# Kernel optimization log

Measured on AMD Instinct MI355X. Metric: run time of the kernel, lower is better.

Reference implementation:

```python
import jax, jax.numpy as jnp
import numpy as np

B, N, E, HID, ED, NH = 2, 10000, 160000, 128, 32, 8
HD = HID // NH  # head_dim = 16
EPS = 1e-5


def setup_inputs() -> dict:
    key = jax.random.key(0)
    ks = jax.random.split(key, 12)
    s = 0.05  # keep pre-tanh activations in a sane range
    return {
        "h": jax.random.normal(ks[0], (B, N, HID), jnp.float32),
        "edge_attr": jax.random.normal(ks[1], (B, E, ED), jnp.float32),
        "edge_index": jax.random.randint(ks[2], (E, 2), 0, N),
        "Wq": jax.random.normal(ks[3], (HID, HID), jnp.float32) * s,
        "bq": jnp.zeros((HID,), jnp.float32),
        "Wk": jax.random.normal(ks[4], (HID, HID), jnp.float32) * s,
        "bk": jnp.zeros((HID,), jnp.float32),
        "Wv": jax.random.normal(ks[5], (HID, HID), jnp.float32) * s,
        "bv": jnp.zeros((HID,), jnp.float32),
        "We": jax.random.normal(ks[6], (HID, ED), jnp.float32) * s,
        "be": jnp.zeros((HID,), jnp.float32),
        "attn_vec": jax.random.normal(ks[7], (NH, HD), jnp.float32) * 0.02,
        "Ws": jax.random.normal(ks[8], (HID, HID), jnp.float32) * s,
        "bs": jnp.zeros((HID,), jnp.float32),
        "Wa": jax.random.normal(ks[9], (HID, HID), jnp.float32) * s,
        "ba": jnp.zeros((HID,), jnp.float32),
        "ln_g": jnp.ones((HID,), jnp.float32),
        "ln_b": jnp.zeros((HID,), jnp.float32),
    }


def reference(h, edge_attr, edge_index, Wq, bq, Wk, bk, Wv, bv, We, be,
              attn_vec, Ws, bs, Wa, ba, ln_g, ln_b):
    src = edge_index[:, 0]
    dst = edge_index[:, 1]
    b, n, hid = h.shape
    e_cnt = src.shape[0]

    h_src = h[:, src, :]  # [B,E,HID]
    h_dst = h[:, dst, :]

    q = (h_dst @ Wq.T + bq).reshape(b, e_cnt, NH, HD)
    k = (h_src @ Wk.T + bk).reshape(b, e_cnt, NH, HD)
    v = (h_src @ Wv.T + bv).reshape(b, e_cnt, NH, HD)
    e = (edge_attr @ We.T + be).reshape(b, e_cnt, NH, HD)

    # GATv2-style scores: [B,E,NH]
    logits = jnp.einsum('behd,hd->beh', jnp.tanh(q + k + e), attn_vec)
    logits = logits / np.float32(np.sqrt(HD))

    # segment softmax over edges grouped by dst node (stable)
    lt = jnp.transpose(logits, (1, 0, 2))  # [E,B,NH]
    mx = jax.ops.segment_max(lt, dst, num_segments=n)  # [N,B,NH]
    ex = jnp.exp(lt - mx[dst])
    den = jax.ops.segment_sum(ex, dst, num_segments=n)
    alpha = jnp.transpose(ex / den[dst], (1, 0, 2))  # [B,E,NH]

    msg = (alpha[..., None] * (v + e)).reshape(b, e_cnt, hid)  # [B,E,HID]
    agg = jax.ops.segment_sum(jnp.transpose(msg, (1, 0, 2)), dst, num_segments=n)
    agg = jnp.transpose(agg, (1, 0, 2))  # [B,N,HID]

    update = (h @ Ws.T + bs) + (agg @ Wa.T + ba)
    x = h + jax.nn.gelu(update, approximate=False)  # dropout is identity in eval

    mu = jnp.mean(x, axis=-1, keepdims=True)
    var = jnp.var(x, axis=-1, keepdims=True)
    return (x - mu) / jnp.sqrt(var + EPS) * ln_g + ln_b
```

## Files before the change

### kernel.cpp

```cpp
#include <hip/hip_runtime.h>
#include <math.h>
#include <stdint.h>

#define B_   2
#define N_   10000
#define E_   160000
#define HID_ 128
#define ED_  32
#define NH_  8
#define HD_  16
#define ROWS_ (B_ * N_)

using half2_t = __attribute__((ext_vector_type(2))) _Float16;
using f16x8   = __attribute__((ext_vector_type(8))) _Float16;
using f32x4   = __attribute__((ext_vector_type(4))) float;

__device__ __forceinline__ half2_t f2h2(float a, float b) {
    return __builtin_bit_cast(half2_t, __builtin_amdgcn_cvt_pkrtz(a, b));
}
__device__ __forceinline__ uint32_t pkh2(float a, float b) {
    return __builtin_bit_cast(uint32_t, __builtin_amdgcn_cvt_pkrtz(a, b));
}


__global__ void hist_kernel(const int* __restrict__ ei, int* __restrict__ deg, int E) {
    int e = blockIdx.x * 256 + threadIdx.x;
    if (e < E) atomicAdd(&deg[ei[2 * e + 1]], 1);
}

__global__ __launch_bounds__(256) void scan_kernel(const int* __restrict__ deg,
                                                   int* __restrict__ off, int N) {
    __shared__ int sums[256];
    int t = threadIdx.x;
    int chunk = (N + 255) / 256;
    int s0 = t * chunk, s1 = min(N, s0 + chunk);
    int s = 0;
    for (int i = s0; i < s1; ++i) s += deg[i];
    sums[t] = s;
    __syncthreads();
    #pragma unroll
    for (int d = 1; d < 256; d <<= 1) {
        int v = (t >= d) ? sums[t - d] : 0;
        __syncthreads();
        sums[t] += v;
        __syncthreads();
    }
    if (t == 255) off[N] = sums[255];
    int run = sums[t] - s;
    for (int i = s0; i < s1; ++i) { off[i] = run; run += deg[i]; }
}

__global__ void fill_kernel(const int* __restrict__ ei, const int* __restrict__ off,
                            int* __restrict__ cursor, int* __restrict__ csr,
                            int* __restrict__ srcs, int E) {
    int e = blockIdx.x * 256 + threadIdx.x;
    if (e < E) {
        int2 se = *(const int2*)(ei + 2 * e);
        int p = atomicAdd(&cursor[se.y], 1);
        int o = off[se.y] + p;
        csr[o] = e;
        srcs[o] = se.x;
    }
}


#define GM 64
#define LDA 68

__global__ __launch_bounds__(256) void qkvs_kernel(
    const float* __restrict__ h,
    const float* __restrict__ Wq, const float* __restrict__ bq,
    const float* __restrict__ Wk, const float* __restrict__ bk,
    const float* __restrict__ Wv, const float* __restrict__ bv,
    const float* __restrict__ Ws, const float* __restrict__ bs,
    const float* __restrict__ ba,
    float* __restrict__ Q, float* __restrict__ KV, float* __restrict__ S)
{
    __shared__ uint32_t As[GM * LDA];
    __shared__ uint32_t Bs[128 * LDA];
    __shared__ float bsm[128];

    int tid = threadIdx.x;
    int lane = tid & 63;
    int wave = tid >> 6;
    int row0 = blockIdx.x * GM;
    int J0 = blockIdx.y * 128;

    if (tid < 128) {
        int J = J0 + tid;
        float v;
        if (J < 128)      v = bq[J];
        else if (J < 256) v = bk[J - 128];
        else if (J < 384) v = bv[J - 256];
        else              v = bs[J - 384] + ba[J - 384];
        bsm[tid] = v;
    }

    for (int f = tid; f < GM * 32; f += 256) {
        int r = f >> 5, c4 = f & 31;
        long row = row0 + r;
        float4 hv = (row < ROWS_) ? *(const float4*)(h + row * HID_ + c4 * 4)
                                  : make_float4(0.f, 0.f, 0.f, 0.f);
        As[r * LDA + c4 * 2]     = pkh2(hv.x, hv.y);
        As[r * LDA + c4 * 2 + 1] = pkh2(hv.z, hv.w);
    }
    for (int f = tid; f < 128 * 32; f += 256) {
        int jr = f >> 5, c4 = f & 31;
        int J = J0 + jr;
        const float* Wp;
        if (J < 128)      Wp = Wq + (long)J * HID_;
        else if (J < 256) Wp = Wk + (long)(J - 128) * HID_;
        else if (J < 384) Wp = Wv + (long)(J - 256) * HID_;
        else              Wp = Ws + (long)(J - 384) * HID_;
        float4 wv = *(const float4*)(Wp + c4 * 4);
        Bs[jr * LDA + c4 * 2]     = pkh2(wv.x, wv.y);
        Bs[jr * LDA + c4 * 2 + 1] = pkh2(wv.z, wv.w);
    }
    __syncthreads();

    f32x4 acc[8];
    #pragma unroll
    for (int nt = 0; nt < 8; ++nt) {
        float c = bsm[nt * 16 + (lane & 15)];
        acc[nt] = (f32x4){ c, c, c, c };
    }

    int ar = wave * 16 + (lane & 15);
    #pragma unroll
    for (int ks = 0; ks < 4; ++ks) {
        f16x8 a = *(const f16x8*)(As + ar * LDA + ks * 16 + (lane >> 4) * 4);
        #pragma unroll
        for (int nt = 0; nt < 8; ++nt) {
            f16x8 b = *(const f16x8*)(Bs + (nt * 16 + (lane & 15)) * LDA + ks * 16 + (lane >> 4) * 4);
            acc[nt] = __builtin_amdgcn_mfma_f32_16x16x32_f16(a, b, acc[nt], 0, 0, 0);
        }
    }

    #pragma unroll
    for (int nt = 0; nt < 8; ++nt) {
        int J = J0 + nt * 16 + (lane & 15);
        long rbase = row0 + wave * 16 + (lane >> 4) * 4;
        #pragma unroll
        for (int r = 0; r < 4; ++r) {
            long row = rbase + r;
            if (row < ROWS_) {
                float v = acc[nt][r];
                if (J < 128)      Q[row * 128 + J] = v;
                else if (J < 256) KV[row * 256 + 2 * (J - 128)] = v;
                else if (J < 384) KV[row * 256 + 2 * (J - 256) + 1] = v;
                else              S[row * 128 + (J - 384)] = v;
            }
        }
    }
}


template <int CTRL>
__device__ __forceinline__ float dpp_add(float x) {
    int y = __builtin_amdgcn_mov_dpp(__float_as_int(x), CTRL, 0xF, 0xF, true);
    return x + __int_as_float(y);
}
__device__ __forceinline__ float hsum16(float p) {
    p = dpp_add<0xB1>(p);
    p = dpp_add<0x4E>(p);
    p = dpp_add<0x141>(p);
    p = dpp_add<0x140>(p);
    return p;
}


#define NPB 4
#define CHUNK 96
#define EAS 20

__global__ __launch_bounds__(128) void node_kernel(
    const float* __restrict__ edge_attr,
    const float* __restrict__ Q, const float* __restrict__ KV,
    const float* __restrict__ We, const float* __restrict__ be,
    const float* __restrict__ attn_vec,
    const int* __restrict__ off, const int* __restrict__ csr,
    const int* __restrict__ srcs,
    float* __restrict__ agg)
{
    int n0 = blockIdx.x * NPB;
    int b  = blockIdx.y;
    int j  = threadIdx.x;
    long bN = (long)b * N_;

    __shared__ int sL[CHUNK];
    __shared__ uint32_t eaL[CHUNK * EAS];

    half2_t we16[16];
    {
        const float4* We4 = (const float4*)(We + (long)j * ED_);
        #pragma unroll
        for (int c = 0; c < 8; ++c) {
            float4 w = We4[c];
            we16[2 * c]     = f2h2(w.x, w.y);
            we16[2 * c + 1] = f2h2(w.z, w.w);
        }
    }
    float bej = be[j];
    float avj = attn_vec[j] * 0.25f;

    float q0 = Q[(bN + n0 + 0) * 128 + j];
    float q1 = Q[(bN + n0 + 1) * 128 + j];
    float q2 = Q[(bN + n0 + 2) * 128 + j];
    float q3 = Q[(bN + n0 + 3) * 128 + j];

    int o0 = off[n0];
    int c1 = off[n0 + 1] - o0, c2 = off[n0 + 2] - o0,
        c3 = off[n0 + 3] - o0, c4_ = off[n0 + 4] - o0;
    int total = c4_;

    const float* eab = edge_attr + (long)b * E_ * ED_;
    const float* KVb = KV + bN * 256;

    float acc0 = 0.f, den0 = 0.f, acc1 = 0.f, den1 = 0.f;
    float acc2 = 0.f, den2 = 0.f, acc3 = 0.f, den3 = 0.f;

    auto edge_body = [&](int i, float qg, float& accg, float& deng) {
        int s = sL[i];
        float2 kv = *(const float2*)(KVb + (long)s * 256 + 2 * j);
        float eja = bej, ejb = 0.f;
        const half2_t* ea = (const half2_t*)(eaL + i * EAS);
        #pragma unroll
        for (int c = 0; c < 8; ++c) {
            eja = __builtin_amdgcn_fdot2(we16[c], ea[c], eja, false);
            ejb = __builtin_amdgcn_fdot2(we16[c + 8], ea[c + 8], ejb, false);
        }
        float ej = eja + ejb;
        float y = qg + kv.x + ej;
        float t = 1.f - 2.f * __builtin_amdgcn_rcpf(__expf(2.f * y) + 1.f);
        float p = hsum16(t * avj);
        float ex = __expf(p);
        deng += ex;
        accg += ex * (kv.y + ej);
    };

    auto range_loop = [&](int lo, int hi, float qg, float& accg, float& deng) {
        int i = lo;
        for (; i + 3 < hi; i += 4) {
            edge_body(i, qg, accg, deng);
            edge_body(i + 1, qg, accg, deng);
            edge_body(i + 2, qg, accg, deng);
            edge_body(i + 3, qg, accg, deng);
        }
        for (; i < hi; ++i) edge_body(i, qg, accg, deng);
    };

    for (int tau = 0; tau < total; tau += CHUNK) {
        int rows = min(total - tau, CHUNK);
        __syncthreads();
        for (int t = j; t < rows; t += 128)
            sL[t] = srcs[o0 + tau + t];
        for (int idx = j; idx < rows * 8; idx += 128) {
            int r = idx >> 3, c = idx & 7;
            int e = csr[o0 + tau + r];
            float4 f = *(const float4*)(eab + (long)e * ED_ + c * 4);
            eaL[r * EAS + 2 * c]     = pkh2(f.x, f.y);
            eaL[r * EAS + 2 * c + 1] = pkh2(f.z, f.w);
        }
        __syncthreads();

        range_loop(max(0 - tau, 0),   min(c1 - tau, rows), q0, acc0, den0);
        range_loop(max(c1 - tau, 0),  min(c2 - tau, rows), q1, acc1, den1);
        range_loop(max(c2 - tau, 0),  min(c3 - tau, rows), q2, acc2, den2);
        range_loop(max(c3 - tau, 0),  min(c4_ - tau, rows), q3, acc3, den3);
    }

    agg[(bN + n0 + 0) * 128 + j] = (c1 > 0)   ? acc0 * __builtin_amdgcn_rcpf(den0) : 0.f;
    agg[(bN + n0 + 1) * 128 + j] = (c2 > c1)  ? acc1 * __builtin_amdgcn_rcpf(den1) : 0.f;
    agg[(bN + n0 + 2) * 128 + j] = (c3 > c2)  ? acc2 * __builtin_amdgcn_rcpf(den2) : 0.f;
    agg[(bN + n0 + 3) * 128 + j] = (c4_ > c3) ? acc3 * __builtin_amdgcn_rcpf(den3) : 0.f;
}


__global__ __launch_bounds__(256) void wa_ln_kernel(
    const float* __restrict__ X,
    const float* __restrict__ Wa,
    const float* __restrict__ S, const float* __restrict__ h,
    const float* __restrict__ ln_g, const float* __restrict__ ln_b,
    float* __restrict__ out)
{
    __shared__ uint32_t As[GM * LDA];
    __shared__ uint32_t Bs[128 * LDA];

    int tid = threadIdx.x;
    int lane = tid & 63;
    int wave = tid >> 6;
    int row0 = blockIdx.x * GM;

    for (int f = tid; f < GM * 32; f += 256) {
        int r = f >> 5, c4 = f & 31;
        long row = row0 + r;
        float4 hv = (row < ROWS_) ? *(const float4*)(X + row * HID_ + c4 * 4)
                                  : make_float4(0.f, 0.f, 0.f, 0.f);
        As[r * LDA + c4 * 2]     = pkh2(hv.x, hv.y);
        As[r * LDA + c4 * 2 + 1] = pkh2(hv.z, hv.w);
    }
    for (int f = tid; f < 128 * 32; f += 256) {
        int jr = f >> 5, c4 = f & 31;
        float4 wv = *(const float4*)(Wa + (long)jr * HID_ + c4 * 4);
        Bs[jr * LDA + c4 * 2]     = pkh2(wv.x, wv.y);
        Bs[jr * LDA + c4 * 2 + 1] = pkh2(wv.z, wv.w);
    }
    __syncthreads();

    f32x4 acc[8];
    #pragma unroll
    for (int nt = 0; nt < 8; ++nt) acc[nt] = (f32x4){ 0.f, 0.f, 0.f, 0.f };

    int ar = wave * 16 + (lane & 15);
    #pragma unroll
    for (int ks = 0; ks < 4; ++ks) {
        f16x8 a = *(const f16x8*)(As + ar * LDA + ks * 16 + (lane >> 4) * 4);
        #pragma unroll
        for (int nt = 0; nt < 8; ++nt) {
            f16x8 b = *(const f16x8*)(Bs + (nt * 16 + (lane & 15)) * LDA + ks * 16 + (lane >> 4) * 4);
            acc[nt] = __builtin_amdgcn_mfma_f32_16x16x32_f16(a, b, acc[nt], 0, 0, 0);
        }
    }

    int lq = lane & 15;
    float gJ[8], bJ[8];
    #pragma unroll
    for (int nt = 0; nt < 8; ++nt) {
        int J = nt * 16 + lq;
        gJ[nt] = ln_g[J];
        bJ[nt] = ln_b[J];
    }
    long rbase = row0 + wave * 16 + (lane >> 4) * 4;
    #pragma unroll
    for (int r = 0; r < 4; ++r) {
        long row = rbase + r;
        if (row < ROWS_) {
            float xv[8];
            float sum = 0.f, sum2 = 0.f;
            #pragma unroll
            for (int nt = 0; nt < 8; ++nt) {
                int J = nt * 16 + lq;
                float upd = acc[nt][r] + S[row * 128 + J];
                float ge = 0.5f * upd * (1.f + erff(upd * 0.70710678118654752f));
                float x = h[row * 128 + J] + ge;
                xv[nt] = x;
                sum += x;
                sum2 += x * x;
            }
            sum = hsum16(sum);
            sum2 = hsum16(sum2);
            float mu = sum * (1.f / 128.f);
            float var = sum2 * (1.f / 128.f) - mu * mu;
            float rs = rsqrtf(var + 1e-5f);
            #pragma unroll
            for (int nt = 0; nt < 8; ++nt)
                out[row * 128 + nt * 16 + lq] = (xv[nt] - mu) * rs * gJ[nt] + bJ[nt];
        }
    }
}


extern "C" void kernel_launch(void* const* d_in, const int* in_sizes, int n_in,
                              void* d_out, int out_size, void* d_ws, size_t ws_size,
                              hipStream_t stream) {
    const float* h         = (const float*)d_in[0];
    const float* edge_attr = (const float*)d_in[1];
    const int*   ei        = (const int*)  d_in[2];
    const float* Wq = (const float*)d_in[3];
    const float* bq = (const float*)d_in[4];
    const float* Wk = (const float*)d_in[5];
    const float* bk = (const float*)d_in[6];
    const float* Wv = (const float*)d_in[7];
    const float* bv = (const float*)d_in[8];
    const float* We = (const float*)d_in[9];
    const float* be = (const float*)d_in[10];
    const float* attn_vec = (const float*)d_in[11];
    const float* Ws = (const float*)d_in[12];
    const float* bs = (const float*)d_in[13];
    const float* Wa = (const float*)d_in[14];
    const float* ba = (const float*)d_in[15];
    const float* ln_g = (const float*)d_in[16];
    const float* ln_b = (const float*)d_in[17];
    float* out = (float*)d_out;

    size_t p = 0;
    auto alloc = [&](size_t bytes) { size_t r = p; p += (bytes + 255) & ~(size_t)255; return r; };
    char* ws = (char*)d_ws;
    float* Q    = (float*)(ws + alloc((size_t)ROWS_ * 128 * 4));
    float* KV   = (float*)(ws + alloc((size_t)ROWS_ * 256 * 4));
    float* S    = (float*)(ws + alloc((size_t)ROWS_ * 128 * 4));
    float* agg  = (float*)(ws + alloc((size_t)ROWS_ * 128 * 4));
    int* dc     = (int*)(ws + alloc((size_t)2 * N_ * 4));
    int* off    = (int*)(ws + alloc((size_t)(N_ + 1) * 4));
    int* csr    = (int*)(ws + alloc((size_t)E_ * 4));
    int* srcs   = (int*)(ws + alloc((size_t)E_ * 4));
    int* deg = dc;
    int* cursor = dc + N_;
    (void)ws_size;

    hipMemsetAsync(dc, 0, (size_t)2 * N_ * 4, stream);
    hist_kernel<<<(E_ + 255) / 256, 256, 0, stream>>>(ei, deg, E_);
    scan_kernel<<<1, 256, 0, stream>>>(deg, off, N_);
    fill_kernel<<<(E_ + 255) / 256, 256, 0, stream>>>(ei, off, cursor, csr, srcs, E_);

    dim3 ggrid((ROWS_ + GM - 1) / GM, 4);
    qkvs_kernel<<<ggrid, 256, 0, stream>>>(h, Wq, bq, Wk, bk, Wv, bv, Ws, bs, ba,
                                           Q, KV, S);

    dim3 grid(N_ / NPB, B_);
    node_kernel<<<grid, 128, 0, stream>>>(edge_attr, Q, KV, We, be, attn_vec,
                                          off, csr, srcs, agg);

    wa_ln_kernel<<<(ROWS_ + GM - 1) / GM, 256, 0, stream>>>(agg, Wa, S, h,
                                                            ln_g, ln_b, out);
}
```

Measured before the change: 177.4 us.

## Store K/V and aggregated messages in fp16 and loop column chunks per block

The projection kernel now writes the interleaved K/V buffer as fp16 instead of fp32, which halves the bytes gathered per edge in the node kernel. The node kernel writes its aggregate in fp16, and the final GEMM copies it straight into shared memory without converting. The QKVS kernel also drops the 4-way column grid: each block loads the h tile once and loops over all four weight chunks, so h is read only once. These changes cut memory traffic but add fp16 rounding to K, V and agg, and each QKVS block now does four times the work with one quarter as many blocks.

```diff
diff --git a/kernel.cpp b/kernel.cpp
--- a/kernel.cpp
+++ b/kernel.cpp
@@ -20,6 +20,9 @@
 }
 __device__ __forceinline__ uint32_t pkh2(float a, float b) {
     return __builtin_bit_cast(uint32_t, __builtin_amdgcn_cvt_pkrtz(a, b));
+}
+__device__ __forceinline__ uint16_t f2h(float v) {
+    return __builtin_bit_cast(uint16_t, (_Float16)v);
 }
 
 
@@ -74,26 +77,24 @@
     const float* __restrict__ Wv, const float* __restrict__ bv,
     const float* __restrict__ Ws, const float* __restrict__ bs,
     const float* __restrict__ ba,
-    float* __restrict__ Q, float* __restrict__ KV, float* __restrict__ S)
+    float* __restrict__ Q, uint16_t* __restrict__ Kv16, float* __restrict__ S)
 {
     __shared__ uint32_t As[GM * LDA];
     __shared__ uint32_t Bs[128 * LDA];
-    __shared__ float bsm[128];
+    __shared__ float bsm[512];
 
     int tid = threadIdx.x;
     int lane = tid & 63;
     int wave = tid >> 6;
     int row0 = blockIdx.x * GM;
-    int J0 = blockIdx.y * 128;
-
-    if (tid < 128) {
-        int J = J0 + tid;
+
+    for (int f = tid; f < 512; f += 256) {
         float v;
-        if (J < 128)      v = bq[J];
-        else if (J < 256) v = bk[J - 128];
-        else if (J < 384) v = bv[J - 256];
-        else              v = bs[J - 384] + ba[J - 384];
-        bsm[tid] = v;
+        if (f < 128)      v = bq[f];
+        else if (f < 256) v = bk[f - 128];
+        else if (f < 384) v = bv[f - 256];
+        else              v = bs[f - 384] + ba[f - 384];
+        bsm[f] = v;
     }
 
     for (int f = tid; f < GM * 32; f += 256) {
@@ -104,51 +105,58 @@
         As[r * LDA + c4 * 2]     = pkh2(hv.x, hv.y);
         As[r * LDA + c4 * 2 + 1] = pkh2(hv.z, hv.w);
     }
-    for (int f = tid; f < 128 * 32; f += 256) {
-        int jr = f >> 5, c4 = f & 31;
-        int J = J0 + jr;
-        const float* Wp;
-        if (J < 128)      Wp = Wq + (long)J * HID_;
-        else if (J < 256) Wp = Wk + (long)(J - 128) * HID_;
-        else if (J < 384) Wp = Wv + (long)(J - 256) * HID_;
-        else              Wp = Ws + (long)(J - 384) * HID_;
-        float4 wv = *(const float4*)(Wp + c4 * 4);
-        Bs[jr * LDA + c4 * 2]     = pkh2(wv.x, wv.y);
-        Bs[jr * LDA + c4 * 2 + 1] = pkh2(wv.z, wv.w);
-    }
-    __syncthreads();
-
-    f32x4 acc[8];
-    #pragma unroll
-    for (int nt = 0; nt < 8; ++nt) {
-        float c = bsm[nt * 16 + (lane & 15)];
-        acc[nt] = (f32x4){ c, c, c, c };
-    }
-
-    int ar = wave * 16 + (lane & 15);
-    #pragma unroll
-    for (int ks = 0; ks < 4; ++ks) {
-        f16x8 a = *(const f16x8*)(As + ar * LDA + ks * 16 + (lane >> 4) * 4);
+
+    int lq = lane & 15;
+    int ar = wave * 16 + lq;
+
+    for (int jc = 0; jc < 4; ++jc) {
+        int J0 = jc * 128;
+        __syncthreads();
+        for (int f = tid; f < 128 * 32; f += 256) {
+            int jr = f >> 5, c4 = f & 31;
+            int J = J0 + jr;
+            const float* Wp;
+            if (J < 128)      Wp = Wq + (long)J * HID_;
+            else if (J < 256) Wp = Wk + (long)(J - 128) * HID_;
+            else if (J < 384) Wp = Wv + (long)(J - 256) * HID_;
+            else              Wp = Ws + (long)(J - 384) * HID_;
+            float4 wv = *(const float4*)(Wp + c4 * 4);
+            Bs[jr * LDA + c4 * 2]     = pkh2(wv.x, wv.y);
+            Bs[jr * LDA + c4 * 2 + 1] = pkh2(wv.z, wv.w);
+        }
+        __syncthreads();
+
+        f32x4 acc[8];
         #pragma unroll
         for (int nt = 0; nt < 8; ++nt) {
-            f16x8 b = *(const f16x8*)(Bs + (nt * 16 + (lane & 15)) * LDA + ks * 16 + (lane >> 4) * 4);
-            acc[nt] = __builtin_amdgcn_mfma_f32_16x16x32_f16(a, b, acc[nt], 0, 0, 0);
-        }
-    }
-
-    #pragma unroll
-    for (int nt = 0; nt < 8; ++nt) {
-        int J = J0 + nt * 16 + (lane & 15);
-        long rbase = row0 + wave * 16 + (lane >> 4) * 4;
-        #pragma unroll
-        for (int r = 0; r < 4; ++r) {
-            long row = rbase + r;
-            if (row < ROWS_) {
-                float v = acc[nt][r];
-                if (J < 128)      Q[row * 128 + J] = v;
-                else if (J < 256) KV[row * 256 + 2 * (J - 128)] = v;
-                else if (J < 384) KV[row * 256 + 2 * (J - 256) + 1] = v;
-                else              S[row * 128 + (J - 384)] = v;
+            float c = bsm[J0 + nt * 16 + lq];
+            acc[nt] = (f32x4){ c, c, c, c };
+        }
+
+        #pragma unroll
+        for (int ks = 0; ks < 4; ++ks) {
+            f16x8 a = *(const f16x8*)(As + ar * LDA + ks * 16 + (lane >> 4) * 4);
+            #pragma unroll
+            for (int nt = 0; nt < 8; ++nt) {
+                f16x8 b = *(const f16x8*)(Bs + (nt * 16 + lq) * LDA + ks * 16 + (lane >> 4) * 4);
+                acc[nt] = __builtin_amdgcn_mfma_f32_16x16x32_f16(a, b, acc[nt], 0, 0, 0);
+            }
+        }
+
+        #pragma unroll
+        for (int nt = 0; nt < 8; ++nt) {
+            int J = J0 + nt * 16 + lq;
+            long rbase = row0 + wave * 16 + (lane >> 4) * 4;
+            #pragma unroll
+            for (int r = 0; r < 4; ++r) {
+                long row = rbase + r;
+                if (row < ROWS_) {
+                    float v = acc[nt][r];
+                    if (J < 128)      Q[row * 128 + J] = v;
+                    else if (J < 256) Kv16[row * 256 + 2 * (J - 128)] = f2h(v);
+                    else if (J < 384) Kv16[row * 256 + 2 * (J - 256) + 1] = f2h(v);
+                    else              S[row * 128 + (J - 384)] = v;
+                }
             }
         }
     }
@@ -175,12 +183,12 @@
 
 __global__ __launch_bounds__(128) void node_kernel(
     const float* __restrict__ edge_attr,
-    const float* __restrict__ Q, const float* __restrict__ KV,
+    const float* __restrict__ Q, const uint32_t* __restrict__ KVp,
     const float* __restrict__ We, const float* __restrict__ be,
     const float* __restrict__ attn_vec,
     const int* __restrict__ off, const int* __restrict__ csr,
     const int* __restrict__ srcs,
-    float* __restrict__ agg)
+    uint16_t* __restrict__ aggh)
 {
     int n0 = blockIdx.x * NPB;
     int b  = blockIdx.y;
@@ -214,14 +222,14 @@
     int total = c4_;
 
     const float* eab = edge_attr + (long)b * E_ * ED_;
-    const float* KVb = KV + bN * 256;
+    const uint32_t* KVb = KVp + bN * 128;
 
     float acc0 = 0.f, den0 = 0.f, acc1 = 0.f, den1 = 0.f;
     float acc2 = 0.f, den2 = 0.f, acc3 = 0.f, den3 = 0.f;
 
     auto edge_body = [&](int i, float qg, float& accg, float& deng) {
         int s = sL[i];
-        float2 kv = *(const float2*)(KVb + (long)s * 256 + 2 * j);
+        half2_t kv = __builtin_bit_cast(half2_t, KVb[(long)s * 128 + j]);
         float eja = bej, ejb = 0.f;
         const half2_t* ea = (const half2_t*)(eaL + i * EAS);
         #pragma unroll
@@ -230,12 +238,12 @@
             ejb = __builtin_amdgcn_fdot2(we16[c + 8], ea[c + 8], ejb, false);
         }
         float ej = eja + ejb;
-        float y = qg + kv.x + ej;
+        float y = qg + (float)kv.x + ej;
         float t = 1.f - 2.f * __builtin_amdgcn_rcpf(__expf(2.f * y) + 1.f);
         float p = hsum16(t * avj);
         float ex = __expf(p);
         deng += ex;
-        accg += ex * (kv.y + ej);
+        accg += ex * ((float)kv.y + ej);
     };
 
     auto range_loop = [&](int lo, int hi, float qg, float& accg, float& deng) {
@@ -269,15 +277,15 @@
         range_loop(max(c3 - tau, 0),  min(c4_ - tau, rows), q3, acc3, den3);
     }
 
-    agg[(bN + n0 + 0) * 128 + j] = (c1 > 0)   ? acc0 * __builtin_amdgcn_rcpf(den0) : 0.f;
-    agg[(bN + n0 + 1) * 128 + j] = (c2 > c1)  ? acc1 * __builtin_amdgcn_rcpf(den1) : 0.f;
-    agg[(bN + n0 + 2) * 128 + j] = (c3 > c2)  ? acc2 * __builtin_amdgcn_rcpf(den2) : 0.f;
-    agg[(bN + n0 + 3) * 128 + j] = (c4_ > c3) ? acc3 * __builtin_amdgcn_rcpf(den3) : 0.f;
+    aggh[(bN + n0 + 0) * 128 + j] = f2h((c1 > 0)   ? acc0 * __builtin_amdgcn_rcpf(den0) : 0.f);
+    aggh[(bN + n0 + 1) * 128 + j] = f2h((c2 > c1)  ? acc1 * __builtin_amdgcn_rcpf(den1) : 0.f);
+    aggh[(bN + n0 + 2) * 128 + j] = f2h((c3 > c2)  ? acc2 * __builtin_amdgcn_rcpf(den2) : 0.f);
+    aggh[(bN + n0 + 3) * 128 + j] = f2h((c4_ > c3) ? acc3 * __builtin_amdgcn_rcpf(den3) : 0.f);
 }
 
 
 __global__ __launch_bounds__(256) void wa_ln_kernel(
-    const float* __restrict__ X,
+    const uint16_t* __restrict__ aggh,
     const float* __restrict__ Wa,
     const float* __restrict__ S, const float* __restrict__ h,
     const float* __restrict__ ln_g, const float* __restrict__ ln_b,
@@ -291,13 +299,13 @@
     int wave = tid >> 6;
     int row0 = blockIdx.x * GM;
 
-    for (int f = tid; f < GM * 32; f += 256) {
-        int r = f >> 5, c4 = f & 31;
+    const uint32_t* Xa = (const uint32_t*)aggh;
+    for (int f = tid; f < GM * 16; f += 256) {
+        int r = f >> 4, c = f & 15;
         long row = row0 + r;
-        float4 hv = (row < ROWS_) ? *(const float4*)(X + row * HID_ + c4 * 4)
-                                  : make_float4(0.f, 0.f, 0.f, 0.f);
-        As[r * LDA + c4 * 2]     = pkh2(hv.x, hv.y);
-        As[r * LDA + c4 * 2 + 1] = pkh2(hv.z, hv.w);
+        uint4 v = (row < ROWS_) ? *(const uint4*)(Xa + row * 64 + c * 4)
+                                : make_uint4(0u, 0u, 0u, 0u);
+        *(uint4*)(&As[r * LDA + c * 4]) = v;
     }
     for (int f = tid; f < 128 * 32; f += 256) {
         int jr = f >> 5, c4 = f & 31;
@@ -311,18 +319,18 @@
     #pragma unroll
     for (int nt = 0; nt < 8; ++nt) acc[nt] = (f32x4){ 0.f, 0.f, 0.f, 0.f };
 
-    int ar = wave * 16 + (lane & 15);
+    int lq = lane & 15;
+    int ar = wave * 16 + lq;
     #pragma unroll
     for (int ks = 0; ks < 4; ++ks) {
         f16x8 a = *(const f16x8*)(As + ar * LDA + ks * 16 + (lane >> 4) * 4);
         #pragma unroll
         for (int nt = 0; nt < 8; ++nt) {
-            f16x8 b = *(const f16x8*)(Bs + (nt * 16 + (lane & 15)) * LDA + ks * 16 + (lane >> 4) * 4);
+            f16x8 b = *(const f16x8*)(Bs + (nt * 16 + lq) * LDA + ks * 16 + (lane >> 4) * 4);
             acc[nt] = __builtin_amdgcn_mfma_f32_16x16x32_f16(a, b, acc[nt], 0, 0, 0);
         }
     }
 
-    int lq = lane & 15;
     float gJ[8], bJ[8];
     #pragma unroll
     for (int nt = 0; nt < 8; ++nt) {
@@ -386,10 +394,10 @@
     size_t p = 0;
     auto alloc = [&](size_t bytes) { size_t r = p; p += (bytes + 255) & ~(size_t)255; return r; };
     char* ws = (char*)d_ws;
-    float* Q    = (float*)(ws + alloc((size_t)ROWS_ * 128 * 4));
-    float* KV   = (float*)(ws + alloc((size_t)ROWS_ * 256 * 4));
-    float* S    = (float*)(ws + alloc((size_t)ROWS_ * 128 * 4));
-    float* agg  = (float*)(ws + alloc((size_t)ROWS_ * 128 * 4));
+    float*    Q    = (float*)(ws + alloc((size_t)ROWS_ * 128 * 4));
+    uint16_t* Kv16 = (uint16_t*)(ws + alloc((size_t)ROWS_ * 256 * 2));
+    float*    S    = (float*)(ws + alloc((size_t)ROWS_ * 128 * 4));
+    uint16_t* aggh = (uint16_t*)(ws + alloc((size_t)ROWS_ * 128 * 2));
     int* dc     = (int*)(ws + alloc((size_t)2 * N_ * 4));
     int* off    = (int*)(ws + alloc((size_t)(N_ + 1) * 4));
     int* csr    = (int*)(ws + alloc((size_t)E_ * 4));
@@ -403,14 +411,13 @@
     scan_kernel<<<1, 256, 0, stream>>>(deg, off, N_);
     fill_kernel<<<(E_ + 255) / 256, 256, 0, stream>>>(ei, off, cursor, csr, srcs, E_);
 
-    dim3 ggrid((ROWS_ + GM - 1) / GM, 4);
-    qkvs_kernel<<<ggrid, 256, 0, stream>>>(h, Wq, bq, Wk, bk, Wv, bv, Ws, bs, ba,
-                                           Q, KV, S);
+    qkvs_kernel<<<(ROWS_ + GM - 1) / GM, 256, 0, stream>>>(h, Wq, bq, Wk, bk, Wv, bv,
+                                                           Ws, bs, ba, Q, Kv16, S);
 
     dim3 grid(N_ / NPB, B_);
-    node_kernel<<<grid, 128, 0, stream>>>(edge_attr, Q, KV, We, be, attn_vec,
-                                          off, csr, srcs, agg);
-
-    wa_ln_kernel<<<(ROWS_ + GM - 1) / GM, 256, 0, stream>>>(agg, Wa, S, h,
+    node_kernel<<<grid, 128, 0, stream>>>(edge_attr, Q, (const uint32_t*)Kv16,
+                                          We, be, attn_vec, off, csr, srcs, aggh);
+
+    wa_ln_kernel<<<(ROWS_ + GM - 1) / GM, 256, 0, stream>>>(aggh, Wa, S, h,
                                                             ln_g, ln_b, out);
 }
```

After: 180.9 us, median of 2. Within noise of the previous version (+2.0%).
